# Kernel optimization log

Hardware: AMD Instinct MI355X
Metric: run time of the kernel (lower is better)

Reference implementation:

```python
import jax, jax.numpy as jnp
import numpy as np

EPS_BN = 1e-5
EPS_COS = 1e-8

N, F_IN, HID, OUT, S, NNZ = 50000, 1024, 256, 280, 5000, 800000


def setup_inputs() -> dict:
    key = jax.random.key(0)
    ks = jax.random.split(key, 20)
    inp = {}
    inp["x"] = jax.random.normal(ks[0], (N, F_IN), jnp.float32)
    inp["y"] = jax.random.normal(ks[1], (S, OUT), jnp.float32)
    inp["adj_rows"] = jax.random.randint(ks[2], (NNZ,), 0, N, jnp.int32)
    inp["adj_cols"] = jax.random.randint(ks[3], (NNZ,), 0, N, jnp.int32)
    inp["adj_vals"] = jax.random.uniform(ks[4], (NNZ,), jnp.float32)
    inp["agg_rows"] = jax.random.randint(ks[5], (N,), 0, S, jnp.int32)
    inp["agg_vals"] = jax.random.uniform(ks[6], (N,), jnp.float32)
    inp["perm"] = jax.random.permutation(ks[7], N).astype(jnp.int32)
    # parameters (kaiming-ish scale)
    def lin(k, fi, fo):
        k1, k2 = jax.random.split(k)
        w = jax.random.normal(k1, (fi, fo), jnp.float32) / np.sqrt(fi)
        b = jax.random.normal(k2, (fo,), jnp.float32) * 0.01
        return w, b
    inp["mlp_W"], inp["mlp_b"] = lin(ks[8], F_IN, HID)
    inp["bn_gamma"] = jnp.ones((HID,), jnp.float32)
    inp["bn_beta"] = jnp.zeros((HID,), jnp.float32)
    inp["hg_W1"], inp["hg_b1"] = lin(ks[9], HID, HID)
    inp["hg_W2"], inp["hg_b2"] = lin(ks[10], HID, HID)
    inp["hg_prelu"] = jnp.float32(0.25)
    inp["pred_W"], inp["pred_b"] = lin(ks[11], HID, OUT)
    inp["dgi_W"], inp["dgi_b"] = lin(ks[12], HID, OUT)
    inp["dgi_prelu"] = jnp.float32(0.25)
    return inp


def _spmm(rows, cols, vals, M, n_out):
    # sparse(H) @ M : gather source rows, scale by edge value, scatter-add to dest
    return jax.ops.segment_sum(vals[:, None] * M[cols], rows, num_segments=n_out)


def _prelu(t, a):
    return jnp.where(t >= 0, t, a * t)


def _leaky(t, s):
    return jnp.where(t >= 0, t, s * t)


def reference(x, y, adj_rows, adj_cols, adj_vals, agg_rows, agg_vals, perm,
              mlp_W, mlp_b, bn_gamma, bn_beta, hg_W1, hg_b1, hg_W2, hg_b2,
              hg_prelu, pred_W, pred_b, dgi_W, dgi_b, dgi_prelu):
    n = x.shape[0]
    s = y.shape[0]
    # mlp: Linear -> LeakyReLU(0.1) -> BatchNorm1d (batch stats, training mode)
    h0 = _leaky(x @ mlp_W + mlp_b, 0.1)
    mu = jnp.mean(h0, axis=0)
    var = jnp.mean((h0 - mu) ** 2, axis=0)  # biased, as torch BN training
    h0 = bn_gamma * (h0 - mu) * jax.lax.rsqrt(var + EPS_BN) + bn_beta
    # HGNN, num_layers=2 (dropout = identity in eval)
    t = _spmm(adj_rows, adj_cols, adj_vals, h0 @ hg_W1 + hg_b1, n)
    t = _prelu(t, hg_prelu)
    t = _spmm(adj_rows, adj_cols, adj_vals, t @ hg_W2 + hg_b2, n)
    h = _leaky(t, 0.01)
    x_prime = _leaky(h @ pred_W + pred_b, 0.01)
    # Xenium: loss = MSE(agg_mtx @ x_prime, y); agg_mtx has one nnz per cell
    agg = jax.ops.segment_sum(agg_vals[:, None] * x_prime, agg_rows, num_segments=s)
    loss = jnp.mean((agg - y) ** 2)
    # DGI (1-layer HGNN with PReLU)
    h1 = _prelu(_spmm(adj_rows, adj_cols, adj_vals, h0 @ dgi_W + dgi_b, n), dgi_prelu)
    c = jnp.mean(h1, axis=0)  # (OUT,)
    h2 = _prelu(_spmm(adj_rows, adj_cols, adj_vals, h0[perm] @ dgi_W + dgi_b, n), dgi_prelu)
    c_norm = jnp.linalg.norm(c)
    def cos(hm):
        return (hm @ c) / jnp.maximum(jnp.linalg.norm(hm, axis=1) * c_norm, EPS_COS)
    loss = loss + jnp.mean(1.0 - cos(h1)) + jnp.mean(jnp.maximum(cos(h2), 0.0))
    return (loss, x_prime)
```

## Files before the change

### kernel.cpp

```cpp
#include <hip/hip_runtime.h>
#include <hip/hip_bf16.h>

#define DEVI __device__ __forceinline__

typedef __attribute__((ext_vector_type(8))) short short8;
typedef __attribute__((ext_vector_type(4))) float float4v;

DEVI float bf2f(__hip_bfloat16 v) { return __bfloat162float(v); }
DEVI float ldbs(const ushort* p, size_t i) { return bf2f(((const __hip_bfloat16*)p)[i]); }
DEVI ushort f2bs(float v) {
    __hip_bfloat16 h = __float2bfloat16(v);
    return *(ushort*)&h;
}
DEVI float bfs2f(short s) {
    ushort u = (ushort)s;
    return bf2f(*(__hip_bfloat16*)&u);
}

DEVI float ldin(const void* p, size_t i, int isf32) {
    return isf32 ? ((const float*)p)[i] : bf2f(((const __hip_bfloat16*)p)[i]);
}
DEVI void stio(void* p, size_t i, float v, int isf32) {
    if (isf32) ((float*)p)[i] = v;
    else ((ushort*)p)[i] = f2bs(v);
}

template <int ACT>
DEVI float act_fn(float v, float alpha) {
    if (ACT == 1) return v >= 0.f ? v : 0.1f * v;
    if (ACT == 2) return v >= 0.f ? v : 0.01f * v;
    if (ACT == 3) return v >= 0.f ? v : alpha * v;
    return v;
}

DEVI float waveRed(float v) {
#pragma unroll
    for (int o = 32; o > 0; o >>= 1) v += __shfl_down(v, o);
    return v;
}

DEVI float blockRed(float v) {
    __shared__ float sm[16];
    int lane = threadIdx.x & 63, w = threadIdx.x >> 6;
    v = waveRed(v);
    if (lane == 0) sm[w] = v;
    __syncthreads();
    if (w == 0) {
        int nw = (blockDim.x + 63) >> 6;
        v = (lane < nw) ? sm[lane] : 0.f;
        v = waveRed(v);
    }
    return v;
}

__global__ void probe_k(const void* __restrict__ x, int* __restrict__ flag) {
    __shared__ int sfails;
    int t = threadIdx.x;
    if (t == 0) sfails = 0;
    __syncthreads();
    const __hip_bfloat16* xb = (const __hip_bfloat16*)x;
    int my = 0;
    for (int i = t; i < 4096; i += 256) {
        float v = bf2f(xb[i]);
        float a = fabsf(v);
        if (!(a <= 64.f) || (v != 0.f && a < 1e-6f)) my++;
    }
    atomicAdd(&sfails, my);
    __syncthreads();
    if (t == 0) flag[0] = (sfails > 409) ? 1 : 0;
}

struct Cvt5 {
    const void* src[5];
    ushort* dst[5];
    int K[5];
    int N[5];
};
__global__ void cvt_all_k(Cvt5 d, const int* __restrict__ flagp) {
    int f32 = flagp[0];
    int seg = blockIdx.y;
    int idx = blockIdx.x * blockDim.x + threadIdx.x;
    int K = d.K[seg], Nc = d.N[seg];
    int total = K * Nc;
    if (idx < total) {
        int k = idx / Nc, n = idx % Nc;
        d.dst[seg][(size_t)n * K + k] = f2bs(ldin(d.src[seg], idx, f32));
    }
}

#define TP 40
template <int AMODE, int ACT, int OMODE>
__global__ __launch_bounds__(256) void mgemm_k(
    const void* __restrict__ A, const ushort* __restrict__ Bt,
    const void* __restrict__ bias, void* __restrict__ outp, ushort* __restrict__ outp2,
    const int* __restrict__ flagp, int M, int K, int Nc, int LDo) {
    __shared__ short As[128 * TP];
    __shared__ short Bs[128 * TP];
    const int f32 = flagp[0];
    const int tid = threadIdx.x;
    const int lane = tid & 63;
    const int l15 = lane & 15;
    const int quad = lane >> 4;
    const int wid = tid >> 6;
    const int mW = (wid >> 1) * 64;
    const int nW = (wid & 1) * 64;
    const int mBase = blockIdx.y * 128;
    const int nBase = blockIdx.x * 128;

    float4v acc[4][4];
#pragma unroll
    for (int i = 0; i < 4; i++)
#pragma unroll
        for (int j = 0; j < 4; j++) acc[i][j] = (float4v){0.f, 0.f, 0.f, 0.f};

    for (int k0 = 0; k0 < K; k0 += 32) {
#pragma unroll
        for (int i = 0; i < 2; i++) {
            int chunk = i * 256 + tid;
            int row = chunk >> 2;
            int c = chunk & 3;
            short8 va = {0, 0, 0, 0, 0, 0, 0, 0};
            int gr = mBase + row;
            if (gr < M) {
                size_t ge = (size_t)gr * K + k0 + c * 8;
                if (AMODE == 1 || !f32) {
                    va = *(const short8*)((const ushort*)A + ge);
                } else {
                    const float* af = (const float*)A + ge;
                    float4v f0 = *(const float4v*)af;
                    float4v f1 = *(const float4v*)(af + 4);
#pragma unroll
                    for (int j = 0; j < 4; j++) va[j] = (short)f2bs(f0[j]);
#pragma unroll
                    for (int j = 0; j < 4; j++) va[4 + j] = (short)f2bs(f1[j]);
                }
            }
            *(short8*)&As[row * TP + c * 8] = va;

            short8 vb = {0, 0, 0, 0, 0, 0, 0, 0};
            int gn = nBase + row;
            if (gn < Nc) vb = *(const short8*)(Bt + (size_t)gn * K + k0 + c * 8);
            *(short8*)&Bs[row * TP + c * 8] = vb;
        }
        __syncthreads();

        short8 af[4], bf[4];
#pragma unroll
        for (int i = 0; i < 4; i++)
            af[i] = *(const short8*)&As[(mW + i * 16 + l15) * TP + quad * 8];
#pragma unroll
        for (int j = 0; j < 4; j++)
            bf[j] = *(const short8*)&Bs[(nW + j * 16 + l15) * TP + quad * 8];
#pragma unroll
        for (int i = 0; i < 4; i++)
#pragma unroll
            for (int j = 0; j < 4; j++)
                acc[i][j] =
                    __builtin_amdgcn_mfma_f32_16x16x32_bf16(af[i], bf[j], acc[i][j], 0, 0, 0);
        __syncthreads();
    }

#pragma unroll
    for (int i = 0; i < 4; i++) {
#pragma unroll
        for (int j = 0; j < 4; j++) {
            int gcn = nBase + nW + j * 16 + l15;
            if (gcn >= Nc) continue;
            float bv = ldin(bias, gcn, f32);
#pragma unroll
            for (int r = 0; r < 4; r++) {
                int grm = mBase + mW + i * 16 + quad * 4 + r;
                if (grm >= M) continue;
                float v = act_fn<ACT>(acc[i][j][r] + bv, 0.f);
                if (OMODE == 1) {
                    stio(outp, 1 + (size_t)grm * Nc + gcn, v, f32);
                    outp2[(size_t)grm * LDo + gcn] = f2bs(v);
                } else {
                    ((ushort*)outp)[(size_t)grm * LDo + gcn] = f2bs(v);
                }
            }
        }
    }
}

__global__ void count_k(const int* __restrict__ rows, int* __restrict__ counts, int nnz) {
    int i = blockIdx.x * blockDim.x + threadIdx.x;
    if (i < nnz) atomicAdd(&counts[rows[i]], 1);
}

__global__ __launch_bounds__(1024) void scan_local_k(const int* __restrict__ counts,
                                                     int* __restrict__ offs,
                                                     int* __restrict__ bsums, int n) {
    __shared__ int sm[1024];
    int t = threadIdx.x;
    int g = blockIdx.x * 1024 + t;
    int v = (g < n) ? counts[g] : 0;
    sm[t] = v;
    __syncthreads();
    for (int d = 1; d < 1024; d <<= 1) {
        int add = (t >= d) ? sm[t - d] : 0;
        __syncthreads();
        sm[t] += add;
        __syncthreads();
    }
    if (g < n) offs[g] = sm[t] - v;
    if (t == 1023) bsums[blockIdx.x] = sm[t];
}

__global__ void scan_bsums_k(int* bsums, int nb) {
    if (threadIdx.x == 0 && blockIdx.x == 0) {
        int acc = 0;
        for (int i = 0; i < nb; i++) {
            int v = bsums[i];
            bsums[i] = acc;
            acc += v;
        }
    }
}

__global__ void scan_add_k(int* __restrict__ offs, const int* __restrict__ bsums, int n, int nnz) {
    int g = blockIdx.x * blockDim.x + threadIdx.x;
    if (g < n) offs[g] += bsums[g >> 10];
    if (g == 0) offs[n] = nnz;
}

__global__ void fill_k(const int* __restrict__ rows, const int* __restrict__ cols,
                       const void* __restrict__ vals, const int* __restrict__ perm,
                       const int* __restrict__ offs, int* __restrict__ cursor,
                       int* __restrict__ cols_s, int* __restrict__ colsp_s,
                       float* __restrict__ vals_s, const int* __restrict__ flagp, int nnz) {
    int e = blockIdx.x * blockDim.x + threadIdx.x;
    if (e < nnz) {
        int r = rows[e];
        int pos = offs[r] + atomicAdd(&cursor[r], 1);
        int c = cols[e];
        cols_s[pos] = c;
        colsp_s[pos] = perm[c];
        vals_s[pos] = ldin(vals, e, flagp[0]);
    }
}

__global__ void fill_s_k(const int* __restrict__ rows, const void* __restrict__ vals,
                         const int* __restrict__ offs, int* __restrict__ cursor,
                         int* __restrict__ idx_s, float* __restrict__ val_s,
                         const int* __restrict__ flagp, int n) {
    int e = blockIdx.x * blockDim.x + threadIdx.x;
    if (e < n) {
        int r = rows[e];
        int pos = offs[r] + atomicAdd(&cursor[r], 1);
        idx_s[pos] = e;
        val_s[pos] = ldin(vals, e, flagp[0]);
    }
}

template <int ACT, bool DUAL>
__global__ __launch_bounds__(256) void spmmv_k(
    const int* __restrict__ offs, const int* __restrict__ cols_s,
    const int* __restrict__ colsp_s, const float* __restrict__ vals_s,
    const void* __restrict__ alpha_p, const int* __restrict__ flagp,
    const ushort* __restrict__ Min, ushort* __restrict__ out1, ushort* __restrict__ out2,
    int Nrow, int F, int LDin) {
    int row = blockIdx.x * 4 + (threadIdx.x >> 6);
    if (row >= Nrow) return;
    int lane = threadIdx.x & 63;
    int half = lane >> 5, l5 = lane & 31;
    int FC = F >> 3;
    bool has1 = (l5 + 32) < FC;
    float alpha = (ACT == 3) ? ldin(alpha_p, 0, flagp[0]) : 0.f;
    int s = offs[row], e = offs[row + 1];
    float a0[8] = {}, a1[8] = {}, b0[8] = {}, b1[8] = {};

    constexpr int DEPTH = DUAL ? 2 : 4;
    int i = s + half;
    for (; i + 2 * (DEPTH - 1) < e; i += 2 * DEPTH) {
        int c[DEPTH];
        float v[DEPTH];
        int cp[DEPTH];
#pragma unroll
        for (int u = 0; u < DEPTH; u++) {
            c[u] = cols_s[i + 2 * u];
            v[u] = vals_s[i + 2 * u];
        }
        if (DUAL) {
#pragma unroll
            for (int u = 0; u < DEPTH; u++) cp[u] = colsp_s[i + 2 * u];
        }
        short8 h0v[DEPTH], h1v[DEPTH], g0v[DEPTH], g1v[DEPTH];
#pragma unroll
        for (int u = 0; u < DEPTH; u++) {
            const ushort* src = Min + (size_t)c[u] * LDin;
            h0v[u] = *(const short8*)(src + l5 * 8);
            if (has1) h1v[u] = *(const short8*)(src + (l5 + 32) * 8);
            if (DUAL) {
                const ushort* srcp = Min + (size_t)cp[u] * LDin;
                g0v[u] = *(const short8*)(srcp + l5 * 8);
                if (has1) g1v[u] = *(const short8*)(srcp + (l5 + 32) * 8);
            }
        }
#pragma unroll
        for (int u = 0; u < DEPTH; u++) {
#pragma unroll
            for (int j = 0; j < 8; j++) a0[j] += v[u] * bfs2f(h0v[u][j]);
            if (has1) {
#pragma unroll
                for (int j = 0; j < 8; j++) a1[j] += v[u] * bfs2f(h1v[u][j]);
            }
            if (DUAL) {
#pragma unroll
                for (int j = 0; j < 8; j++) b0[j] += v[u] * bfs2f(g0v[u][j]);
                if (has1) {
#pragma unroll
                    for (int j = 0; j < 8; j++) b1[j] += v[u] * bfs2f(g1v[u][j]);
                }
            }
        }
    }
    for (; i < e; i += 2) {
        float v = vals_s[i];
        int c = cols_s[i];
        const ushort* src = Min + (size_t)c * LDin;
        short8 h = *(const short8*)(src + l5 * 8);
#pragma unroll
        for (int j = 0; j < 8; j++) a0[j] += v * bfs2f(h[j]);
        if (has1) {
            short8 h2 = *(const short8*)(src + (l5 + 32) * 8);
#pragma unroll
            for (int j = 0; j < 8; j++) a1[j] += v * bfs2f(h2[j]);
        }
        if (DUAL) {
            int cp = colsp_s[i];
            const ushort* srcp = Min + (size_t)cp * LDin;
            short8 g = *(const short8*)(srcp + l5 * 8);
#pragma unroll
            for (int j = 0; j < 8; j++) b0[j] += v * bfs2f(g[j]);
            if (has1) {
                short8 g2 = *(const short8*)(srcp + (l5 + 32) * 8);
#pragma unroll
                for (int j = 0; j < 8; j++) b1[j] += v * bfs2f(g2[j]);
            }
        }
    }
#pragma unroll
    for (int j = 0; j < 8; j++) {
        a0[j] += __shfl_xor(a0[j], 32);
        if (has1) a1[j] += __shfl_xor(a1[j], 32);
        if (DUAL) {
            b0[j] += __shfl_xor(b0[j], 32);
            if (has1) b1[j] += __shfl_xor(b1[j], 32);
        }
    }
    if (half == 0) {
        short8 o;
        size_t base = (size_t)row * F;
#pragma unroll
        for (int j = 0; j < 8; j++) o[j] = (short)f2bs(act_fn<ACT>(a0[j], alpha));
        *(short8*)(out1 + base + l5 * 8) = o;
        if (has1) {
#pragma unroll
            for (int j = 0; j < 8; j++) o[j] = (short)f2bs(act_fn<ACT>(a1[j], alpha));
            *(short8*)(out1 + base + (l5 + 32) * 8) = o;
        }
        if (DUAL) {
#pragma unroll
            for (int j = 0; j < 8; j++) o[j] = (short)f2bs(act_fn<ACT>(b0[j], alpha));
            *(short8*)(out2 + base + l5 * 8) = o;
            if (has1) {
#pragma unroll
                for (int j = 0; j < 8; j++) o[j] = (short)f2bs(act_fn<ACT>(b1[j], alpha));
                *(short8*)(out2 + base + (l5 + 32) * 8) = o;
            }
        }
    }
}

__global__ __launch_bounds__(256) void aggmse_k(
    const int* __restrict__ soffs, const int* __restrict__ sidx, const float* __restrict__ sval,
    const ushort* __restrict__ xp, const void* __restrict__ y, const int* __restrict__ flagp,
    float* __restrict__ lacc, int S, int F, int LDxp) {
    int srow = blockIdx.x * 4 + (threadIdx.x >> 6);
    int lane = threadIdx.x & 63;
    int half = lane >> 5, l5 = lane & 31;
    int FC = F >> 3;
    bool has1 = (l5 + 32) < FC;
    float a0[8] = {}, a1[8] = {};
    if (srow < S) {
        int s = soffs[srow], e = soffs[srow + 1];
        for (int i = s + half; i < e; i += 2) {
            float v = sval[i];
            int n = sidx[i];
            const ushort* src = xp + (size_t)n * LDxp;
            short8 h = *(const short8*)(src + l5 * 8);
#pragma unroll
            for (int j = 0; j < 8; j++) a0[j] += v * bfs2f(h[j]);
            if (has1) {
                short8 h2 = *(const short8*)(src + (l5 + 32) * 8);
#pragma unroll
                for (int j = 0; j < 8; j++) a1[j] += v * bfs2f(h2[j]);
            }
        }
    }
#pragma unroll
    for (int j = 0; j < 8; j++) {
        a0[j] += __shfl_xor(a0[j], 32);
        if (has1) a1[j] += __shfl_xor(a1[j], 32);
    }
    float ss = 0.f;
    if (srow < S && half == 0) {
        int f32 = flagp[0];
        size_t base = (size_t)srow * F;
#pragma unroll
        for (int j = 0; j < 8; j++) {
            float d = a0[j] - ldin(y, base + l5 * 8 + j, f32);
            ss += d * d;
        }
        if (has1) {
#pragma unroll
            for (int j = 0; j < 8; j++) {
                float d = a1[j] - ldin(y, base + (l5 + 32) * 8 + j, f32);
                ss += d * d;
            }
        }
    }
    ss = blockRed(ss);
    if (threadIdx.x == 0) atomicAdd(&lacc[0], ss);
}

__global__ __launch_bounds__(256) void bn_stats_k(const ushort* __restrict__ h,
                                                  float* __restrict__ sum,
                                                  float* __restrict__ sumsq, int nrows, int rpb) {
    int c = threadIdx.x;
    int rs = blockIdx.x * rpb;
    int re = min(rs + rpb, nrows);
    float s = 0.f, s2 = 0.f;
    int H = blockDim.x;
    for (int r = rs; r < re; r++) {
        float v = ldbs(h, (size_t)r * H + c);
        s += v;
        s2 += v * v;
    }
    atomicAdd(&sum[c], s);
    atomicAdd(&sumsq[c], s2);
}

__global__ void bn_final_k(const float* __restrict__ sum, const float* __restrict__ sumsq,
                           const void* __restrict__ gamma, const void* __restrict__ beta,
                           float* __restrict__ scale, float* __restrict__ shift,
                           const int* __restrict__ flagp, int nrows) {
    int c = threadIdx.x;
    int f32 = flagp[0];
    float mu = sum[c] / nrows;
    float var = sumsq[c] / nrows - mu * mu;
    float sc = ldin(gamma, c, f32) * rsqrtf(var + 1e-5f);
    scale[c] = sc;
    shift[c] = ldin(beta, c, f32) - mu * sc;
}

__global__ __launch_bounds__(256) void bn_apply_k(ushort* __restrict__ h,
                                                  const float* __restrict__ scale,
                                                  const float* __restrict__ shift, int total8,
                                                  int H) {
    int idx = blockIdx.x * 256 + threadIdx.x;
    if (idx >= total8) return;
    size_t base = (size_t)idx * 8;
    int c = (int)(base % H);
    short8 v = *(short8*)(h + base);
    short8 o;
#pragma unroll
    for (int j = 0; j < 8; j++) o[j] = (short)f2bs(bfs2f(v[j]) * scale[c + j] + shift[c + j]);
    *(short8*)(h + base) = o;
}

__global__ __launch_bounds__(320) void colsum_k(const ushort* __restrict__ h,
                                                float* __restrict__ accum, int nrows, int F,
                                                int rpb) {
    int f = threadIdx.x;
    if (f >= F) return;
    int rs = blockIdx.x * rpb;
    int re = min(rs + rpb, nrows);
    float s = 0.f;
    for (int r = rs; r < re; r++) s += ldbs(h, (size_t)r * F + f);
    atomicAdd(&accum[f], s);
}

__global__ __launch_bounds__(320) void cfinal_k(const float* __restrict__ accum,
                                                float* __restrict__ c, float* __restrict__ cnorm,
                                                int N, int F) {
    int f = threadIdx.x;
    float v = 0.f;
    if (f < F) {
        v = accum[f] / N;
        c[f] = v;
    }
    float s2 = blockRed(v * v);
    if (threadIdx.x == 0) cnorm[0] = sqrtf(s2);
}

template <int MODE>
__global__ __launch_bounds__(256) void cos_k(const ushort* __restrict__ h,
                                             const float* __restrict__ c,
                                             const float* __restrict__ cnorm,
                                             float* __restrict__ acc, int N, int F) {
    int gw = (blockIdx.x * blockDim.x + threadIdx.x) >> 6;
    int lane = threadIdx.x & 63;
    int nw = (gridDim.x * blockDim.x) >> 6;
    float cn = cnorm[0];
    float s = 0.f;
    for (int row = gw; row < N; row += nw) {
        float dot = 0.f, nsq = 0.f;
        for (int f = lane; f < F; f += 64) {
            float v = ldbs(h, (size_t)row * F + f);
            dot += v * c[f];
            nsq += v * v;
        }
#pragma unroll
        for (int o = 32; o > 0; o >>= 1) {
            dot += __shfl_down(dot, o);
            nsq += __shfl_down(nsq, o);
        }
        if (lane == 0) {
            float cosv = dot / fmaxf(sqrtf(nsq) * cn, 1e-8f);
            s += (MODE == 1) ? fmaxf(cosv, 0.f) : cosv;
        }
    }
    s = blockRed(s);
    if (threadIdx.x == 0) atomicAdd(acc, s);
}

__global__ void final_k(const float* __restrict__ lacc, void* __restrict__ dout,
                        const int* __restrict__ flagp, int SOUT, int N) {
    if (threadIdx.x == 0 && blockIdx.x == 0) {
        float loss = lacc[0] / SOUT + (1.f - lacc[1] / N) + lacc[2] / N;
        stio(dout, 0, loss, flagp[0]);
    }
}

extern "C" void kernel_launch(void* const* d_in, const int* in_sizes, int n_in,
                              void* d_out, int out_size, void* d_ws, size_t ws_size,
                              hipStream_t stream) {
    const void* x = d_in[0];
    const void* y = d_in[1];
    const int* adj_rows = (const int*)d_in[2];
    const int* adj_cols = (const int*)d_in[3];
    const void* adj_vals = d_in[4];
    const int* agg_rows = (const int*)d_in[5];
    const void* agg_vals = d_in[6];
    const int* perm = (const int*)d_in[7];
    const void* mlp_W = d_in[8];
    const void* mlp_b = d_in[9];
    const void* bn_gamma = d_in[10];
    const void* bn_beta = d_in[11];
    const void* hg_W1 = d_in[12];
    const void* hg_b1 = d_in[13];
    const void* hg_W2 = d_in[14];
    const void* hg_b2 = d_in[15];
    const void* hg_prelu = d_in[16];
    const void* pred_W = d_in[17];
    const void* pred_b = d_in[18];
    const void* dgi_W = d_in[19];
    const void* dgi_b = d_in[20];
    const void* dgi_prelu = d_in[21];

    const int N = in_sizes[5];
    const int NNZ = in_sizes[2];
    const int F_IN = in_sizes[0] / N;
    const int HID = in_sizes[9];
    const int OUT = in_sizes[18];
    const int S = in_sizes[1] / OUT;

    const int LDP = (OUT + 63) & ~63;

    char* w = (char*)d_ws;
    size_t off = 0;
    auto alloc = [&](size_t b) -> char* {
        char* p = w + off;
        off += (b + 255) & ~(size_t)255;
        return p;
    };
    ushort* h0_bf = (ushort*)alloc((size_t)N * HID * 2);
    ushort* zA_bf = (ushort*)alloc((size_t)N * LDP * 2);
    ushort* zB_bf = (ushort*)alloc((size_t)N * OUT * 2);
    ushort* h2_bf = (ushort*)alloc((size_t)N * OUT * 2);
    ushort* xp_ws = zA_bf;
    ushort* mlpWt = (ushort*)alloc((size_t)HID * F_IN * 2);
    ushort* hgW1t = (ushort*)alloc((size_t)HID * HID * 2);
    ushort* hgW2t = (ushort*)alloc((size_t)HID * HID * 2);
    ushort* predWt = (ushort*)alloc((size_t)OUT * HID * 2);
    ushort* dgiWt = (ushort*)alloc((size_t)OUT * HID * 2);
    int* offs = (int*)alloc((size_t)(N + 1) * 4);
    int nbscan = (N + 1023) / 1024;
    int* bsums = (int*)alloc((size_t)nbscan * 4);
    int* cols_s = (int*)alloc((size_t)NNZ * 4);
    int* colsp_s = (int*)alloc((size_t)NNZ * 4);
    float* vals_s = (float*)alloc((size_t)NNZ * 4);
    int* soffs = (int*)alloc((size_t)(S + 1) * 4);
    int nbscan_s = (S + 1023) / 1024;
    int* sbsums = (int*)alloc((size_t)nbscan_s * 4);
    int* sidx = (int*)alloc((size_t)N * 4);
    float* sval = (float*)alloc((size_t)N * 4);
    float* bn_scale = (float*)alloc((size_t)HID * 4);
    float* bn_shift = (float*)alloc((size_t)HID * 4);
    float* c_vec = (float*)alloc((size_t)OUT * 4);
    float* cnorm = (float*)alloc(4);
    int* dflag = (int*)alloc(16);
    char* zero_base = w + off;
    int* counts = (int*)alloc((size_t)N * 4);
    int* cursor = (int*)alloc((size_t)N * 4);
    int* scnt = (int*)alloc((size_t)S * 4);
    int* scursor = (int*)alloc((size_t)S * 4);
    float* bn_sum = (float*)alloc((size_t)HID * 4);
    float* bn_sumsq = (float*)alloc((size_t)HID * 4);
    float* c_acc = (float*)alloc((size_t)OUT * 4);
    float* lacc = (float*)alloc(16);
    size_t zero_bytes = (w + off) - zero_base;
    hipMemsetAsync(zero_base, 0, zero_bytes, stream);

    probe_k<<<1, 256, 0, stream>>>(x, dflag);

    Cvt5 cv;
    cv.src[0] = mlp_W;  cv.dst[0] = mlpWt;  cv.K[0] = F_IN; cv.N[0] = HID;
    cv.src[1] = hg_W1;  cv.dst[1] = hgW1t;  cv.K[1] = HID;  cv.N[1] = HID;
    cv.src[2] = hg_W2;  cv.dst[2] = hgW2t;  cv.K[2] = HID;  cv.N[2] = HID;
    cv.src[3] = pred_W; cv.dst[3] = predWt; cv.K[3] = HID;  cv.N[3] = OUT;
    cv.src[4] = dgi_W;  cv.dst[4] = dgiWt;  cv.K[4] = HID;  cv.N[4] = OUT;
    cvt_all_k<<<dim3((F_IN * HID + 255) / 256, 5), 256, 0, stream>>>(cv, dflag);

    count_k<<<(NNZ + 255) / 256, 256, 0, stream>>>(adj_rows, counts, NNZ);
    scan_local_k<<<nbscan, 1024, 0, stream>>>(counts, offs, bsums, N);
    scan_bsums_k<<<1, 64, 0, stream>>>(bsums, nbscan);
    scan_add_k<<<(N + 255) / 256, 256, 0, stream>>>(offs, bsums, N, NNZ);
    fill_k<<<(NNZ + 255) / 256, 256, 0, stream>>>(adj_rows, adj_cols, adj_vals, perm, offs,
                                                  cursor, cols_s, colsp_s, vals_s, dflag, NNZ);
    count_k<<<(N + 255) / 256, 256, 0, stream>>>(agg_rows, scnt, N);
    scan_local_k<<<nbscan_s, 1024, 0, stream>>>(scnt, soffs, sbsums, S);
    scan_bsums_k<<<1, 64, 0, stream>>>(sbsums, nbscan_s);
    scan_add_k<<<(S + 255) / 256, 256, 0, stream>>>(soffs, sbsums, S, N);
    fill_s_k<<<(N + 255) / 256, 256, 0, stream>>>(agg_rows, agg_vals, soffs, scursor, sidx, sval,
                                                  dflag, N);

    const int MT = (N + 127) / 128;
    const int SPB = (N + 3) / 4;
    mgemm_k<0, 1, 0><<<dim3((HID + 127) / 128, MT), 256, 0, stream>>>(
        x, mlpWt, mlp_b, h0_bf, nullptr, dflag, N, F_IN, HID, HID);
    bn_stats_k<<<(N + 127) / 128, HID, 0, stream>>>(h0_bf, bn_sum, bn_sumsq, N, 128);
    bn_final_k<<<1, HID, 0, stream>>>(bn_sum, bn_sumsq, bn_gamma, bn_beta, bn_scale, bn_shift,
                                      dflag, N);
    {
        int total8 = (N * HID) / 8;
        bn_apply_k<<<(total8 + 255) / 256, 256, 0, stream>>>(h0_bf, bn_scale, bn_shift, total8,
                                                             HID);
    }

    mgemm_k<1, 0, 0><<<dim3((HID + 127) / 128, MT), 256, 0, stream>>>(
        h0_bf, hgW1t, hg_b1, zA_bf, nullptr, dflag, N, HID, HID, HID);
    spmmv_k<3, false><<<SPB, 256, 0, stream>>>(offs, cols_s, colsp_s, vals_s, hg_prelu, dflag,
                                               zA_bf, zB_bf, nullptr, N, HID, HID);
    mgemm_k<1, 0, 0><<<dim3((HID + 127) / 128, MT), 256, 0, stream>>>(
        zB_bf, hgW2t, hg_b2, zA_bf, nullptr, dflag, N, HID, HID, HID);
    spmmv_k<2, false><<<SPB, 256, 0, stream>>>(offs, cols_s, colsp_s, vals_s, nullptr, dflag,
                                               zA_bf, zB_bf, nullptr, N, HID, HID);

    mgemm_k<1, 2, 1><<<dim3((OUT + 127) / 128, MT), 256, 0, stream>>>(
        zB_bf, predWt, pred_b, d_out, xp_ws, dflag, N, HID, OUT, LDP);
    aggmse_k<<<(S + 3) / 4, 256, 0, stream>>>(soffs, sidx, sval, xp_ws, y, dflag, lacc, S, OUT,
                                              LDP);

    mgemm_k<1, 0, 0><<<dim3((OUT + 127) / 128, MT), 256, 0, stream>>>(
        h0_bf, dgiWt, dgi_b, zA_bf, nullptr, dflag, N, HID, OUT, LDP);
    spmmv_k<3, true><<<SPB, 256, 0, stream>>>(offs, cols_s, colsp_s, vals_s, dgi_prelu, dflag,
                                              zA_bf, zB_bf, h2_bf, N, OUT, LDP);
    colsum_k<<<(N + 127) / 128, 320, 0, stream>>>(zB_bf, c_acc, N, OUT, 128);
    cfinal_k<<<1, 320, 0, stream>>>(c_acc, c_vec, cnorm, N, OUT);
    cos_k<0><<<256, 256, 0, stream>>>(zB_bf, c_vec, cnorm, &lacc[1], N, OUT);
    cos_k<1><<<256, 256, 0, stream>>>(h2_bf, c_vec, cnorm, &lacc[2], N, OUT);

    final_k<<<1, 64, 0, stream>>>(lacc, d_out, dflag, S * OUT, N);
}
```

Before: 1.357 ms.

## Prefetch next GEMM K-tile into registers and batch gathers in aggregation kernel

The GEMM main loop now loads the next K-tile from global memory into registers while MFMAs run on the current shared-memory tile, then commits it to LDS after a barrier. This overlaps global latency with compute but raises register pressure. The aggregation kernel also unrolls its gather loop by four and issues all row loads before accumulating, which increases memory-level parallelism.

Result: faster. 1.282 ms (-5.5%).

```diff
diff --git a/kernel.cpp b/kernel.cpp
--- a/kernel.cpp
+++ b/kernel.cpp
@@ -113,35 +113,62 @@
 #pragma unroll
         for (int j = 0; j < 4; j++) acc[i][j] = (float4v){0.f, 0.f, 0.f, 0.f};
 
-    for (int k0 = 0; k0 < K; k0 += 32) {
+    short8 sa[2], sb[2];
+    float4v fa[2][2];
+
+    auto issue_tile = [&](int k0) {
 #pragma unroll
         for (int i = 0; i < 2; i++) {
             int chunk = i * 256 + tid;
             int row = chunk >> 2;
             int c = chunk & 3;
-            short8 va = {0, 0, 0, 0, 0, 0, 0, 0};
             int gr = mBase + row;
-            if (gr < M) {
-                size_t ge = (size_t)gr * K + k0 + c * 8;
-                if (AMODE == 1 || !f32) {
-                    va = *(const short8*)((const ushort*)A + ge);
+            int gn = nBase + row;
+            size_t geA = (size_t)gr * K + k0 + c * 8;
+            if (AMODE == 0 && f32) {
+                if (gr < M) {
+                    const float* af = (const float*)A + geA;
+                    fa[i][0] = *(const float4v*)af;
+                    fa[i][1] = *(const float4v*)(af + 4);
                 } else {
-                    const float* af = (const float*)A + ge;
-                    float4v f0 = *(const float4v*)af;
-                    float4v f1 = *(const float4v*)(af + 4);
-#pragma unroll
-                    for (int j = 0; j < 4; j++) va[j] = (short)f2bs(f0[j]);
-#pragma unroll
-                    for (int j = 0; j < 4; j++) va[4 + j] = (short)f2bs(f1[j]);
+                    fa[i][0] = (float4v){0.f, 0.f, 0.f, 0.f};
+                    fa[i][1] = (float4v){0.f, 0.f, 0.f, 0.f};
                 }
+            } else {
+                sa[i] = (gr < M) ? *(const short8*)((const ushort*)A + geA)
+                                 : (short8){0, 0, 0, 0, 0, 0, 0, 0};
+            }
+            sb[i] = (gn < Nc) ? *(const short8*)(Bt + (size_t)gn * K + k0 + c * 8)
+                              : (short8){0, 0, 0, 0, 0, 0, 0, 0};
+        }
+    };
+
+    auto commit_tile = [&]() {
+#pragma unroll
+        for (int i = 0; i < 2; i++) {
+            int chunk = i * 256 + tid;
+            int row = chunk >> 2;
+            int c = chunk & 3;
+            short8 va;
+            if (AMODE == 0 && f32) {
+#pragma unroll
+                for (int j = 0; j < 4; j++) va[j] = (short)f2bs(fa[i][0][j]);
+#pragma unroll
+                for (int j = 0; j < 4; j++) va[4 + j] = (short)f2bs(fa[i][1][j]);
+            } else {
+                va = sa[i];
             }
             *(short8*)&As[row * TP + c * 8] = va;
-
-            short8 vb = {0, 0, 0, 0, 0, 0, 0, 0};
-            int gn = nBase + row;
-            if (gn < Nc) vb = *(const short8*)(Bt + (size_t)gn * K + k0 + c * 8);
-            *(short8*)&Bs[row * TP + c * 8] = vb;
-        }
+            *(short8*)&Bs[row * TP + c * 8] = sb[i];
+        }
+    };
+
+    const int nk = K >> 5;
+    issue_tile(0);
+    for (int t = 0; t < nk; ++t) {
+        __syncthreads();
+        commit_tile();
+        if (t + 1 < nk) issue_tile((t + 1) << 5);
         __syncthreads();
 
         short8 af[4], bf[4];
@@ -157,7 +184,6 @@
             for (int j = 0; j < 4; j++)
                 acc[i][j] =
                     __builtin_amdgcn_mfma_f32_16x16x32_bf16(af[i], bf[j], acc[i][j], 0, 0, 0);
-        __syncthreads();
     }
 
 #pragma unroll
@@ -385,7 +411,34 @@
     float a0[8] = {}, a1[8] = {};
     if (srow < S) {
         int s = soffs[srow], e = soffs[srow + 1];
-        for (int i = s + half; i < e; i += 2) {
+        constexpr int DEPTH = 4;
+        int i = s + half;
+        for (; i + 2 * (DEPTH - 1) < e; i += 2 * DEPTH) {
+            int n[DEPTH];
+            float v[DEPTH];
+#pragma unroll
+            for (int u = 0; u < DEPTH; u++) {
+                n[u] = sidx[i + 2 * u];
+                v[u] = sval[i + 2 * u];
+            }
+            short8 h0v[DEPTH], h1v[DEPTH];
+#pragma unroll
+            for (int u = 0; u < DEPTH; u++) {
+                const ushort* src = xp + (size_t)n[u] * LDxp;
+                h0v[u] = *(const short8*)(src + l5 * 8);
+                if (has1) h1v[u] = *(const short8*)(src + (l5 + 32) * 8);
+            }
+#pragma unroll
+            for (int u = 0; u < DEPTH; u++) {
+#pragma unroll
+                for (int j = 0; j < 8; j++) a0[j] += v[u] * bfs2f(h0v[u][j]);
+                if (has1) {
+#pragma unroll
+                    for (int j = 0; j < 8; j++) a1[j] += v[u] * bfs2f(h1v[u][j]);
+                }
+            }
+        }
+        for (; i < e; i += 2) {
             float v = sval[i];
             int n = sidx[i];
             const ushort* src = xp + (size_t)n * LDxp;
```
